# Kernel tuning notes

Hardware: AMD Instinct MI355X
Metric: run time of the kernel (lower is better)

## Reference

```python
import jax, jax.numpy as jnp
import numpy as np

TWO_PI = 2.0 * np.pi


def setup_inputs() -> dict:
    key = jax.random.key(0)
    k1, k2 = jax.random.split(key)
    B, N, F = 1, 4096, 4096
    query_points = jax.random.normal(k1, (B, N, 3), dtype=jnp.float32)
    face_coord = jax.random.normal(k2, (B, F, 3, 3), dtype=jnp.float32)
    return {"query_points": query_points, "face_coord": face_coord}


def _winding(query_points, face_coord):
    # query_points: [B, N, 3]; face_coord: [B, F, 3, 3]
    # Per-pair vectors from query point to each triangle vertex: [B, N, F, 3]
    qp = query_points[:, :, None, :]  # [B, N, 1, 3]
    a = face_coord[:, None, :, 0, :] - qp
    b = face_coord[:, None, :, 1, :] - qp
    c = face_coord[:, None, :, 2, :] - qp

    det = jnp.sum(a * jnp.cross(b, c), axis=-1)          # [B, N, F]
    na = jnp.linalg.norm(a, axis=-1)
    nb = jnp.linalg.norm(b, axis=-1)
    nc = jnp.linalg.norm(c, axis=-1)
    ab = jnp.sum(a * b, axis=-1)
    bc = jnp.sum(b * c, axis=-1)
    ac = jnp.sum(a * c, axis=-1)

    denom = na * nb * nc + bc * na + ac * nb + ab * nc
    solid_angle_2 = jnp.arctan2(det, denom)              # [B, N, F]
    # Sum solid angles over all faces, normalize by 2*pi -> winding number/occupancy
    return jnp.sum(solid_angle_2, axis=-1) / TWO_PI      # [B, N]


def reference(query_points, face_coord):
    return _winding(query_points, face_coord)
```

## Files before the change

### kernel.cpp

```cpp
#include <hip/hip_runtime.h>
#include <math.h>

#define N_Q 4096
#define N_F 4096
#define QPT 2
#define QBLK (256 * QPT)
#define FSPLIT 256
#define FT (N_F / FSPLIT)
#define INV_2PI 0.15915494309189535f

__device__ __forceinline__ float fast_atan2f(float y, float x) {
    const float pi   = 3.14159265358979f;
    const float pi_2 = 1.57079632679490f;
    float ax = fabsf(x), ay = fabsf(y);
    float mx = fmaxf(ax, ay), mn = fminf(ax, ay);
    float t = mn * __builtin_amdgcn_rcpf(mx);
    t = (mx == 0.0f) ? 0.0f : t;
    float s = t * t;
    float p =              -0.0117212f;
    p = fmaf(p, s,  0.05265332f);
    p = fmaf(p, s, -0.11643287f);
    p = fmaf(p, s,  0.19354346f);
    p = fmaf(p, s, -0.33262347f);
    p = fmaf(p, s,  0.99997726f);
    float r = p * t;
    r = (ay > ax) ? (pi_2 - r) : r;
    r = (x < 0.0f) ? (pi - r) : r;
    return copysignf(r, y);
}

__device__ __forceinline__ float pair_term(
    float qx, float qy, float qz,
    float v0, float v1, float v2, float v3, float v4,
    float v5, float v6, float v7, float v8)
{
    const float ax = v0 - qx, ay = v1 - qy, az = v2 - qz;
    const float bx = v3 - qx, by = v4 - qy, bz = v5 - qz;
    const float cx = v6 - qx, cy = v7 - qy, cz = v8 - qz;

    const float ux = fmaf(by, cz, -bz * cy);
    const float uy = fmaf(bz, cx, -bx * cz);
    const float uz = fmaf(bx, cy, -by * cx);
    const float det = fmaf(ax, ux, fmaf(ay, uy, az * uz));

    const float na = __builtin_amdgcn_sqrtf(fmaf(ax, ax, fmaf(ay, ay, az * az)));
    const float nb = __builtin_amdgcn_sqrtf(fmaf(bx, bx, fmaf(by, by, bz * bz)));
    const float nc = __builtin_amdgcn_sqrtf(fmaf(cx, cx, fmaf(cy, cy, cz * cz)));

    const float ab = fmaf(ax, bx, fmaf(ay, by, az * bz));
    const float bc = fmaf(bx, cx, fmaf(by, cy, bz * cz));
    const float ac = fmaf(ax, cx, fmaf(ay, cy, az * cz));

    const float denom = fmaf(na * nb, nc, fmaf(bc, na, fmaf(ac, nb, ab * nc)));
    return fast_atan2f(det, denom);
}

__global__ __launch_bounds__(256) void winding_kernel(
    const float* __restrict__ qp,
    const float* __restrict__ fc,
    float* __restrict__ out)
{
    const int q0 = blockIdx.x * QBLK + threadIdx.x;
    const int q1 = q0 + 256;
    const int f0 = blockIdx.y * FT;

    const float q0x = qp[q0*3+0], q0y = qp[q0*3+1], q0z = qp[q0*3+2];
    const float q1x = qp[q1*3+0], q1y = qp[q1*3+1], q1z = qp[q1*3+2];

    float s0 = 0.0f, s1 = 0.0f;
    #pragma unroll 4
    for (int f = 0; f < FT; ++f) {
        const float* v = fc + (size_t)(f0 + f) * 9;
        const float v0 = v[0], v1 = v[1], v2 = v[2];
        const float v3 = v[3], v4 = v[4], v5 = v[5];
        const float v6 = v[6], v7 = v[7], v8 = v[8];

        s0 += pair_term(q0x, q0y, q0z, v0, v1, v2, v3, v4, v5, v6, v7, v8);
        s1 += pair_term(q1x, q1y, q1z, v0, v1, v2, v3, v4, v5, v6, v7, v8);
    }

    atomicAdd(&out[q0], s0 * INV_2PI);
    atomicAdd(&out[q1], s1 * INV_2PI);
}

extern "C" void kernel_launch(void* const* d_in, const int* in_sizes, int n_in,
                              void* d_out, int out_size, void* d_ws, size_t ws_size,
                              hipStream_t stream) {
    const float* qp = (const float*)d_in[0];
    const float* fc = (const float*)d_in[1];
    float* out = (float*)d_out;

    hipMemsetAsync(out, 0, (size_t)out_size * sizeof(float), stream);

    dim3 grid(N_Q / QBLK, FSPLIT);
    dim3 block(256);
    winding_kernel<<<grid, block, 0, stream>>>(qp, fc, out);
}
```

Measured before the change: 32.51 us.

## Precompute per-face constants in shared memory and expand pair terms algebraically

```diff
diff --git a/kernel.cpp b/kernel.cpp
--- a/kernel.cpp
+++ b/kernel.cpp
@@ -5,7 +5,7 @@
 #define N_F 4096
 #define QPT 2
 #define QBLK (256 * QPT)
-#define FSPLIT 256
+#define FSPLIT 128
 #define FT (N_F / FSPLIT)
 #define INV_2PI 0.15915494309189535f
 
@@ -14,8 +14,8 @@
     const float pi_2 = 1.57079632679490f;
     float ax = fabsf(x), ay = fabsf(y);
     float mx = fmaxf(ax, ay), mn = fminf(ax, ay);
+    mx = fmaxf(mx, 1e-30f);
     float t = mn * __builtin_amdgcn_rcpf(mx);
-    t = (mx == 0.0f) ? 0.0f : t;
     float s = t * t;
     float p =              -0.0117212f;
     p = fmaf(p, s,  0.05265332f);
@@ -30,26 +30,21 @@
 }
 
 __device__ __forceinline__ float pair_term(
-    float qx, float qy, float qz,
-    float v0, float v1, float v2, float v3, float v4,
-    float v5, float v6, float v7, float v8)
+    float qx, float qy, float qz, float th,
+    float4 A, float4 B, float4 C, float4 Nv, float4 K)
 {
-    const float ax = v0 - qx, ay = v1 - qy, az = v2 - qz;
-    const float bx = v3 - qx, by = v4 - qy, bz = v5 - qz;
-    const float cx = v6 - qx, cy = v7 - qy, cz = v8 - qz;
+    const float da  = fmaf(-qx, A.x, fmaf(-qy, A.y, fmaf(-qz, A.z, th)));
+    const float db  = fmaf(-qx, B.x, fmaf(-qy, B.y, fmaf(-qz, B.z, th)));
+    const float dc  = fmaf(-qx, C.x, fmaf(-qy, C.y, fmaf(-qz, C.z, th)));
+    const float det = fmaf(-qx, Nv.x, fmaf(-qy, Nv.y, fmaf(-qz, Nv.z, Nv.w)));
 
-    const float ux = fmaf(by, cz, -bz * cy);
-    const float uy = fmaf(bz, cx, -bx * cz);
-    const float uz = fmaf(bx, cy, -by * cx);
-    const float det = fmaf(ax, ux, fmaf(ay, uy, az * uz));
+    const float na = __builtin_amdgcn_sqrtf(fmaf(2.0f, da, A.w));
+    const float nb = __builtin_amdgcn_sqrtf(fmaf(2.0f, db, B.w));
+    const float nc = __builtin_amdgcn_sqrtf(fmaf(2.0f, dc, C.w));
 
-    const float na = __builtin_amdgcn_sqrtf(fmaf(ax, ax, fmaf(ay, ay, az * az)));
-    const float nb = __builtin_amdgcn_sqrtf(fmaf(bx, bx, fmaf(by, by, bz * bz)));
-    const float nc = __builtin_amdgcn_sqrtf(fmaf(cx, cx, fmaf(cy, cy, cz * cz)));
-
-    const float ab = fmaf(ax, bx, fmaf(ay, by, az * bz));
-    const float bc = fmaf(bx, cx, fmaf(by, cy, bz * cz));
-    const float ac = fmaf(ax, cx, fmaf(ay, cy, az * cz));
+    const float ab = K.x + (da + db);
+    const float bc = K.y + (db + dc);
+    const float ac = K.z + (da + dc);
 
     const float denom = fmaf(na * nb, nc, fmaf(bc, na, fmaf(ac, nb, ab * nc)));
     return fast_atan2f(det, denom);
@@ -60,23 +55,51 @@
     const float* __restrict__ fc,
     float* __restrict__ out)
 {
-    const int q0 = blockIdx.x * QBLK + threadIdx.x;
+    __shared__ float  raw[FT * 9];
+    __shared__ float4 cst[FT][5];
+
+    const int tid = threadIdx.x;
+
+    for (int i = tid; i < FT * 9; i += 256)
+        raw[i] = fc[(size_t)blockIdx.y * FT * 9 + i];
+    __syncthreads();
+
+    if (tid < FT) {
+        const float* v = &raw[tid * 9];
+        const float ax = v[0], ay = v[1], az = v[2];
+        const float bx = v[3], by = v[4], bz = v[5];
+        const float cx = v[6], cy = v[7], cz = v[8];
+        const float ux = by*cz - bz*cy, uy = bz*cx - bx*cz, uz = bx*cy - by*cx;
+        const float vx = cy*az - cz*ay, vy = cz*ax - cx*az, vz = cx*ay - cy*ax;
+        const float wx = ay*bz - az*by, wy = az*bx - ax*bz, wz = ax*by - ay*bx;
+        const float D  = ax*ux + ay*uy + az*uz;
+        cst[tid][0] = make_float4(ax, ay, az, ax*ax + ay*ay + az*az);
+        cst[tid][1] = make_float4(bx, by, bz, bx*bx + by*by + bz*bz);
+        cst[tid][2] = make_float4(cx, cy, cz, cx*cx + cy*cy + cz*cz);
+        cst[tid][3] = make_float4(ux + vx + wx, uy + vy + wy, uz + vz + wz, D);
+        cst[tid][4] = make_float4(ax*bx + ay*by + az*bz,
+                                  bx*cx + by*cy + bz*cz,
+                                  ax*cx + ay*cy + az*cz, 0.0f);
+    }
+    __syncthreads();
+
+    const int q0 = blockIdx.x * QBLK + tid;
     const int q1 = q0 + 256;
-    const int f0 = blockIdx.y * FT;
-
     const float q0x = qp[q0*3+0], q0y = qp[q0*3+1], q0z = qp[q0*3+2];
     const float q1x = qp[q1*3+0], q1y = qp[q1*3+1], q1z = qp[q1*3+2];
+    const float th0 = 0.5f * fmaf(q0x, q0x, fmaf(q0y, q0y, q0z * q0z));
+    const float th1 = 0.5f * fmaf(q1x, q1x, fmaf(q1y, q1y, q1z * q1z));
 
     float s0 = 0.0f, s1 = 0.0f;
     #pragma unroll 4
     for (int f = 0; f < FT; ++f) {
-        const float* v = fc + (size_t)(f0 + f) * 9;
-        const float v0 = v[0], v1 = v[1], v2 = v[2];
-        const float v3 = v[3], v4 = v[4], v5 = v[5];
-        const float v6 = v[6], v7 = v[7], v8 = v[8];
-
-        s0 += pair_term(q0x, q0y, q0z, v0, v1, v2, v3, v4, v5, v6, v7, v8);
-        s1 += pair_term(q1x, q1y, q1z, v0, v1, v2, v3, v4, v5, v6, v7, v8);
+        const float4 A  = cst[f][0];
+        const float4 B  = cst[f][1];
+        const float4 C  = cst[f][2];
+        const float4 Nv = cst[f][3];
+        const float4 K  = cst[f][4];
+        s0 += pair_term(q0x, q0y, q0z, th0, A, B, C, Nv, K);
+        s1 += pair_term(q1x, q1y, q1z, th1, A, B, C, Nv, K);
     }
 
     atomicAdd(&out[q0], s0 * INV_2PI);
```

Result: faster. 28.64 us (-11.9%).

## Merge four atan2 terms via complex products and restructure face distribution

Applied to the files above, without the earlier changes.

```diff
diff --git a/kernel.cpp b/kernel.cpp
--- a/kernel.cpp
+++ b/kernel.cpp
@@ -3,10 +3,11 @@
 
 #define N_Q 4096
 #define N_F 4096
-#define QPT 2
-#define QBLK (256 * QPT)
-#define FSPLIT 256
-#define FT (N_F / FSPLIT)
+#define NBLK 512
+#define QPW 2
+#define TF 256
+#define NT (N_F / TF)
+#define REC 12
 #define INV_2PI 0.15915494309189535f
 
 __device__ __forceinline__ float fast_atan2f(float y, float x) {
@@ -14,8 +15,8 @@
     const float pi_2 = 1.57079632679490f;
     float ax = fabsf(x), ay = fabsf(y);
     float mx = fmaxf(ax, ay), mn = fminf(ax, ay);
+    mx = fmaxf(mx, 1e-30f);
     float t = mn * __builtin_amdgcn_rcpf(mx);
-    t = (mx == 0.0f) ? 0.0f : t;
     float s = t * t;
     float p =              -0.0117212f;
     p = fmaf(p, s,  0.05265332f);
@@ -29,10 +30,21 @@
     return copysignf(r, y);
 }
 
-__device__ __forceinline__ float pair_term(
+__device__ __forceinline__ void merge_angle(
+    float y1, float x1, float y2, float x2,
+    float& ym, float& xm, float& w)
+{
+    ym = fmaf(y1, x2, y2 * x1);
+    xm = fmaf(-y1, y2, x1 * x2);
+    const float c = copysignf(1.0f, y1) + copysignf(1.0f, y2);
+    w += (ym * c < 0.0f) ? 0.5f * c : 0.0f;
+}
+
+__device__ __forceinline__ void raw_dn(
     float qx, float qy, float qz,
     float v0, float v1, float v2, float v3, float v4,
-    float v5, float v6, float v7, float v8)
+    float v5, float v6, float v7, float v8,
+    float& det, float& den)
 {
     const float ax = v0 - qx, ay = v1 - qy, az = v2 - qz;
     const float bx = v3 - qx, by = v4 - qy, bz = v5 - qz;
@@ -41,7 +53,7 @@
     const float ux = fmaf(by, cz, -bz * cy);
     const float uy = fmaf(bz, cx, -bx * cz);
     const float uz = fmaf(bx, cy, -by * cx);
-    const float det = fmaf(ax, ux, fmaf(ay, uy, az * uz));
+    det = fmaf(ax, ux, fmaf(ay, uy, az * uz));
 
     const float na = __builtin_amdgcn_sqrtf(fmaf(ax, ax, fmaf(ay, ay, az * az)));
     const float nb = __builtin_amdgcn_sqrtf(fmaf(bx, bx, fmaf(by, by, bz * bz)));
@@ -51,8 +63,7 @@
     const float bc = fmaf(bx, cx, fmaf(by, cy, bz * cz));
     const float ac = fmaf(ax, cx, fmaf(ay, cy, az * cz));
 
-    const float denom = fmaf(na * nb, nc, fmaf(bc, na, fmaf(ac, nb, ab * nc)));
-    return fast_atan2f(det, denom);
+    den = fmaf(na * nb, nc, fmaf(bc, na, fmaf(ac, nb, ab * nc)));
 }
 
 __global__ __launch_bounds__(256) void winding_kernel(
@@ -60,27 +71,92 @@
     const float* __restrict__ fc,
     float* __restrict__ out)
 {
-    const int q0 = blockIdx.x * QBLK + threadIdx.x;
-    const int q1 = q0 + 256;
-    const int f0 = blockIdx.y * FT;
+    __shared__ __align__(16) float buf[2][TF * REC];
+    __shared__ float aux[2][TF];
+
+    const int tid  = threadIdx.x;
+    const int lane = tid & 63;
+    const int wid  = tid >> 6;
+    const int q0   = blockIdx.x * 8 + wid * QPW;
+    const int q1   = q0 + 1;
 
     const float q0x = qp[q0*3+0], q0y = qp[q0*3+1], q0z = qp[q0*3+2];
     const float q1x = qp[q1*3+0], q1y = qp[q1*3+1], q1z = qp[q1*3+2];
 
-    float s0 = 0.0f, s1 = 0.0f;
-    #pragma unroll 4
-    for (int f = 0; f < FT; ++f) {
-        const float* v = fc + (size_t)(f0 + f) * 9;
-        const float v0 = v[0], v1 = v[1], v2 = v[2];
-        const float v3 = v[3], v4 = v[4], v5 = v[5];
-        const float v6 = v[6], v7 = v[7], v8 = v[8];
+    {
+        const float* src = fc + (size_t)tid * 9;
+        float r[9];
+        #pragma unroll
+        for (int k = 0; k < 9; ++k) r[k] = src[k];
+        float4* b4 = (float4*)buf[0];
+        b4[tid*3+0] = make_float4(r[0], r[1], r[2], r[3]);
+        b4[tid*3+1] = make_float4(r[4], r[5], r[6], r[7]);
+        aux[0][tid] = r[8];
+    }
+    __syncthreads();
 
-        s0 += pair_term(q0x, q0y, q0z, v0, v1, v2, v3, v4, v5, v6, v7, v8);
-        s1 += pair_term(q1x, q1y, q1z, v0, v1, v2, v3, v4, v5, v6, v7, v8);
+    float s0 = 0.0f, w0 = 0.0f, s1 = 0.0f, w1 = 0.0f;
+
+    for (int t = 0; t < NT; ++t) {
+        const int cur = t & 1;
+
+        float r[9];
+        if (t + 1 < NT) {
+            const float* src = fc + ((size_t)(t + 1) * TF + tid) * 9;
+            #pragma unroll
+            for (int k = 0; k < 9; ++k) r[k] = src[k];
+        }
+
+        const float4* b4 = (const float4*)buf[cur];
+        float d0[4], n0[4], d1[4], n1[4];
+        #pragma unroll
+        for (int i = 0; i < 4; ++i) {
+            const int fi = lane + (i << 6);
+            const float4 p0 = b4[fi*3+0];
+            const float4 p1 = b4[fi*3+1];
+            const float v8 = aux[cur][fi];
+            raw_dn(q0x,q0y,q0z, p0.x,p0.y,p0.z,p0.w, p1.x,p1.y,p1.z,p1.w, v8,
+                   d0[i], n0[i]);
+            raw_dn(q1x,q1y,q1z, p0.x,p0.y,p0.z,p0.w, p1.x,p1.y,p1.z,p1.w, v8,
+                   d1[i], n1[i]);
+        }
+
+        {
+            float ya,xa,yb,xb,Y,X;
+            merge_angle(d0[0],n0[0], d0[1],n0[1], ya,xa, w0);
+            merge_angle(d0[2],n0[2], d0[3],n0[3], yb,xb, w0);
+            merge_angle(ya,xa, yb,xb, Y,X, w0);
+            s0 += fast_atan2f(Y, X);
+        }
+        {
+            float ya,xa,yb,xb,Y,X;
+            merge_angle(d1[0],n1[0], d1[1],n1[1], ya,xa, w1);
+            merge_angle(d1[2],n1[2], d1[3],n1[3], yb,xb, w1);
+            merge_angle(ya,xa, yb,xb, Y,X, w1);
+            s1 += fast_atan2f(Y, X);
+        }
+
+        if (t + 1 < NT) {
+            __syncthreads();
+            float4* wb = (float4*)buf[cur ^ 1];
+            wb[tid*3+0] = make_float4(r[0], r[1], r[2], r[3]);
+            wb[tid*3+1] = make_float4(r[4], r[5], r[6], r[7]);
+            aux[cur ^ 1][tid] = r[8];
+            __syncthreads();
+        }
     }
 
-    atomicAdd(&out[q0], s0 * INV_2PI);
-    atomicAdd(&out[q1], s1 * INV_2PI);
+    #pragma unroll
+    for (int m = 1; m < 64; m <<= 1) {
+        s0 += __shfl_xor(s0, m);
+        w0 += __shfl_xor(w0, m);
+        s1 += __shfl_xor(s1, m);
+        w1 += __shfl_xor(w1, m);
+    }
+    if (lane == 0) {
+        out[q0] = fmaf(s0, INV_2PI, w0);
+        out[q1] = fmaf(s1, INV_2PI, w1);
+    }
 }
 
 extern "C" void kernel_launch(void* const* d_in, const int* in_sizes, int n_in,
@@ -90,9 +166,5 @@
     const float* fc = (const float*)d_in[1];
     float* out = (float*)d_out;
 
-    hipMemsetAsync(out, 0, (size_t)out_size * sizeof(float), stream);
-
-    dim3 grid(N_Q / QBLK, FSPLIT);
-    dim3 block(256);
-    winding_kernel<<<grid, block, 0, stream>>>(qp, fc, out);
+    winding_kernel<<<dim3(NBLK), dim3(256), 0, stream>>>(qp, fc, out);
 }
```

Result: faster. 30.36 us (-6.6%).
